# Performance work log

Measured on AMD Instinct MI355X. Metric: run time of the kernel, lower is better.

## Reference

```python
import jax, jax.numpy as jnp
import numpy as np

# Clockwork RNN config (mirrors global args in the original script)
N1, N2, N3 = 16, 8, 8          # len(args.x1/x2/x3)
MULT = 8
DX = N1 + N2 + N3               # 32
D1, D2, D3 = N1*MULT, N2*MULT, N3*MULT  # 128, 64, 64
DH1 = DX * MULT                 # 256
DH2 = 512
DY = 4
T = 192
B = 512
R2, R3 = 2, 4                   # args.x2_rate, args.x3_rate


def _schedule_masks():
    # feat[j]: which input features are consumed at step j (zeroing a feature
    # is equivalent to slicing the matching rows of w_x).
    # blk[j]: which hidden units are updated at step j (others keep old value).
    feat = np.zeros((T, DX), np.float32)
    blk = np.zeros((T, DH1), np.bool_)
    for j in range(T):
        if (j + 1) % R2 == 0:
            if (j + 1) % R3 == 0:
                feat[j, :] = 1.0
                blk[j, :] = True
            else:
                feat[j, :N1 + N2] = 1.0
                blk[j, :D1 + D2] = True
        else:
            feat[j, :N1] = 1.0
            blk[j, :D1] = True
    return jnp.asarray(feat), jnp.asarray(blk)


def setup_inputs() -> dict:
    key = jax.random.key(0)
    ks = jax.random.split(key, 8)
    std = 1.0 / np.sqrt(DH1)
    u = lambda k, shape, s: jax.random.uniform(k, shape, jnp.float32, -s, s)
    return {
        "x": jax.random.normal(ks[0], (B, T, DX), jnp.float32),
        "w_x": u(ks[1], (DY, DX, DH1), std),
        "w_h": u(ks[2], (DY, DH1, DH1), std),
        "b": u(ks[3], (DY, DH1), std),
        "W1": u(ks[4], (DY, DH1, DH2), 1.0 / np.sqrt(DH1)),
        "b1": u(ks[5], (DY, DH2), 1.0 / np.sqrt(DH1)),
        "W2": u(ks[6], (DY, DH2), 1.0 / np.sqrt(DH2)),
        "b2": u(ks[7], (DY,), 1.0 / np.sqrt(DH2)),
    }


def reference(x, w_x, w_h, b, W1, b1, W2, b2):
    feat, blk = _schedule_masks()

    def step(h, inp):
        xj, fm, bm = inp              # xj:[B,DX] fm:[DX] bm:[DH1]
        xin = xj * fm                 # masked features == sliced w_x rows
        cand = jnp.tanh(
            jnp.einsum("bx,yxd->byd", xin, w_x)
            + jnp.einsum("byd,yde->bye", h, w_h)
            + b
        )                             # [B,DY,DH1]
        h = jnp.where(bm, cand, h)    # only scheduled blocks update
        return h, None

    h0 = jnp.zeros((x.shape[0], DY, DH1), x.dtype)
    hT, _ = jax.lax.scan(step, h0, (jnp.swapaxes(x, 0, 1), feat, blk))
    hid = jax.nn.relu(jnp.einsum("byd,ydh->byh", hT, W1) + b1)
    y = jnp.einsum("byh,yh->by", hid, W2) + b2   # [B,DY]
    return y
```

## Files before the change

### kernel.cpp

```cpp
#include <hip/hip_runtime.h>
#include <math.h>


#define TT    192
#define DXX   32
#define DH1   256
#define DH2   512
#define NY    4
#define ROWS8 8
#define PADK  264

typedef _Float16 f16x8 __attribute__((ext_vector_type(8)));
typedef __attribute__((ext_vector_type(4))) float f32x4;
typedef __attribute__((ext_vector_type(2))) int   i32x2;
typedef __attribute__((ext_vector_type(4))) int   i32x4;

template<int N> struct IC { static constexpr int v = N; };

__device__ __forceinline__ unsigned pkrtz(float a, float b) {
    unsigned d;
    asm("v_cvt_pkrtz_f16_f32 %0, %1, %2" : "=v"(d) : "v"(a), "v"(b));
    return d;
}
__device__ __forceinline__ unsigned short f16bits(_Float16 h) {
    union { _Float16 f; unsigned short u; } c; c.f = h; return c.u;
}
__device__ __forceinline__ float fast_tanh(float v) {
    float t = __builtin_amdgcn_exp2f(v * 2.885390081777927f);
    return fmaf(-2.f, __builtin_amdgcn_rcpf(t + 1.f), 1.f);
}

__global__ __launch_bounds__(512, 2) void cwrnn_mfma8(
    const float* __restrict__ x,
    const float* __restrict__ w_x,
    const float* __restrict__ w_h,
    const float* __restrict__ bias,
    const float* __restrict__ W1,
    const float* __restrict__ b1,
    const float* __restrict__ W2,
    const float* __restrict__ b2,
    float* __restrict__ out)
{
    __shared__ _Float16 hb[2][ROWS8 * PADK];
    __shared__ float red[8][ROWS8];
    __shared__ float scratch[DXX * DH1];

    const int t    = threadIdx.x;
    const int lane = t & 63;
    const int w    = t >> 6;
    const int r    = lane & 15;
    const int rb   = r & 7;
    const int q    = lane >> 4;
    const int y    = blockIdx.x & 3;
    const int b0   = (blockIdx.x >> 2) * ROWS8;

    const float* wx_g = w_x + (size_t)y * DXX * DH1;
    const float* wh_g = w_h + (size_t)y * DH1 * DH1;

    for (int i = t; i < ROWS8 * PADK; i += 512) hb[0][i] = (_Float16)0.f;

    f16x8 wxf[2];
    for (int i = t * 4; i < DXX * DH1; i += 2048)
        *(f32x4*)&scratch[i] = *(const f32x4*)&wx_g[i];
    __syncthreads();
    #pragma unroll
    for (int m = 0; m < 2; ++m) {
        f16x8 vh;
        #pragma unroll
        for (int jj = 0; jj < 8; ++jj)
            vh[jj] = (_Float16)scratch[(q * 8 + jj) * DH1 + ((m * 8 + w) << 4) + r];
        wxf[m] = vh;
    }
    __syncthreads();

    f16x8 whf[8][2];
    #pragma unroll
    for (int kt = 0; kt < 8; ++kt) {
        for (int i = t * 4; i < 32 * DH1; i += 2048)
            *(f32x4*)&scratch[i] = *(const f32x4*)&wh_g[kt * 32 * DH1 + i];
        __syncthreads();
        #pragma unroll
        for (int m = 0; m < 2; ++m) {
            f16x8 vh;
            #pragma unroll
            for (int jj = 0; jj < 8; ++jj)
                vh[jj] = (_Float16)scratch[(q * 8 + jj) * DH1 + ((m * 8 + w) << 4) + r];
            whf[kt][m] = vh;
        }
        __syncthreads();
    }

    f32x4 bias4[2];
    #pragma unroll
    for (int m = 0; m < 2; ++m)
        #pragma unroll
        for (int rr = 0; rr < 4; ++rr)
            bias4[m][rr] = bias[y * DH1 + ((m * 8 + w) << 4) + q * 4 + rr];

    const _Float16* hrd[2] = { &hb[0][rb * PADK] + q * 8,
                               &hb[1][rb * PADK] + q * 8 };
    _Float16* hwr[2] = { &hb[0][rb * PADK + w * 16 + q * 4],
                         &hb[1][rb * PADK + w * 16 + q * 4] };

    const float* xrow = x + (size_t)(b0 + rb) * TT * DXX + q * 8;
    f32x4 cxa = *(const f32x4*)&xrow[0];
    f32x4 cxb = *(const f32x4*)&xrow[4];

    auto body = [&](int j, auto SC, int cur) {
        constexpr int S  = SC.v;
        constexpr int NF = (S == 0) ? 16 : (S == 1) ? 24 : 32;
        const bool m1act = (S == 2) || (S == 1 && w < 4);

        const int jn = (j + 1 < TT) ? j + 1 : j;
        const f32x4 pxa = *(const f32x4*)&xrow[jn * DXX];
        const f32x4 pxb = *(const f32x4*)&xrow[jn * DXX + 4];

        f16x8 xf;
        if (q * 8 < NF) {
            union { i32x4 i; f16x8 h; } ux;
            ux.i = (i32x4){ (int)pkrtz(cxa[0], cxa[1]), (int)pkrtz(cxa[2], cxa[3]),
                            (int)pkrtz(cxb[0], cxb[1]), (int)pkrtz(cxb[2], cxb[3]) };
            xf = ux.h;
        } else {
            xf = (f16x8)(_Float16)0.f;
        }

        const _Float16* hp = hrd[cur];

        f32x4 a0a = bias4[0], a0b = {0,0,0,0};
        f32x4 a1a = bias4[1], a1b = {0,0,0,0};

        #pragma unroll
        for (int kt = 0; kt < 4; ++kt) {
            const f16x8 hv0 = *(const f16x8*)(hp + kt * 32);
            const f16x8 hv1 = *(const f16x8*)(hp + (kt + 4) * 32);
            a0a = __builtin_amdgcn_mfma_f32_16x16x32_f16(whf[kt][0], hv0, a0a, 0, 0, 0);
            a0b = __builtin_amdgcn_mfma_f32_16x16x32_f16(whf[kt + 4][0], hv1, a0b, 0, 0, 0);
            if (m1act) {
                a1a = __builtin_amdgcn_mfma_f32_16x16x32_f16(whf[kt][1], hv0, a1a, 0, 0, 0);
                a1b = __builtin_amdgcn_mfma_f32_16x16x32_f16(whf[kt + 4][1], hv1, a1b, 0, 0, 0);
            }
        }
        a0b = __builtin_amdgcn_mfma_f32_16x16x32_f16(wxf[0], xf, a0b, 0, 0, 0);
        if (m1act)
            a1b = __builtin_amdgcn_mfma_f32_16x16x32_f16(wxf[1], xf, a1b, 0, 0, 0);

        {
            const f32x4 s = a0a + a0b;
            const unsigned short h0 = f16bits((_Float16)fast_tanh(s[0]));
            const unsigned short h1 = f16bits((_Float16)fast_tanh(s[1]));
            const unsigned short h2 = f16bits((_Float16)fast_tanh(s[2]));
            const unsigned short h3 = f16bits((_Float16)fast_tanh(s[3]));
            if (r < 8) {
                *(i32x2*)(hwr[cur ^ 1]) =
                    (i32x2){ (int)(h0 | ((unsigned)h1 << 16)),
                             (int)(h2 | ((unsigned)h3 << 16)) };
            }
        }
        if (m1act) {
            const f32x4 s = a1a + a1b;
            const unsigned short h0 = f16bits((_Float16)fast_tanh(s[0]));
            const unsigned short h1 = f16bits((_Float16)fast_tanh(s[1]));
            const unsigned short h2 = f16bits((_Float16)fast_tanh(s[2]));
            const unsigned short h3 = f16bits((_Float16)fast_tanh(s[3]));
            if (r < 8) {
                *(i32x2*)(hwr[cur ^ 1] + 128) =
                    (i32x2){ (int)(h0 | ((unsigned)h1 << 16)),
                             (int)(h2 | ((unsigned)h3 << 16)) };
            }
        } else {
            if (r < 8)
                *(i32x2*)(hwr[cur ^ 1] + 128) = *(const i32x2*)(hwr[cur] + 128);
        }
        __syncthreads();
        cxa = pxa; cxb = pxb;
    };

    for (int j = 0; j < TT; j += 4) {
        body(j + 0, IC<0>{}, 0);
        body(j + 1, IC<1>{}, 1);
        body(j + 2, IC<0>{}, 0);
        body(j + 3, IC<2>{}, 1);
    }

    float* hT = scratch;
    for (int i = t; i < DH1 * ROWS8; i += 512) {
        const int row = i & 7, k = i >> 3;
        hT[k * ROWS8 + row] = (float)hb[0][row * PADK + k];
    }
    __syncthreads();

    const float* W1_g = W1 + (size_t)y * DH1 * DH2;
    float a0[8];
    #pragma unroll
    for (int m = 0; m < 8; ++m) a0[m] = 0.f;
    for (int k = 0; k < DH1; ++k) {
        const float wv = W1_g[(size_t)k * DH2 + t];
        const f32x4 hA = *(const f32x4*)&hT[k * ROWS8];
        const f32x4 hB = *(const f32x4*)&hT[k * ROWS8 + 4];
        a0[0] += hA[0] * wv; a0[1] += hA[1] * wv;
        a0[2] += hA[2] * wv; a0[3] += hA[3] * wv;
        a0[4] += hB[0] * wv; a0[5] += hB[1] * wv;
        a0[6] += hB[2] * wv; a0[7] += hB[3] * wv;
    }
    {
        const float b1v = b1[y * DH2 + t];
        const float w2v = W2[y * DH2 + t];
        float p[8];
        #pragma unroll
        for (int m = 0; m < 8; ++m)
            p[m] = fmaxf(a0[m] + b1v, 0.f) * w2v;
        #pragma unroll
        for (int m = 0; m < 8; ++m) {
            float v = p[m];
            for (int off = 32; off > 0; off >>= 1) v += __shfl_down(v, off);
            if (lane == 0) red[w][m] = v;
        }
    }
    __syncthreads();
    if (t < ROWS8) {
        float s = b2[y];
        #pragma unroll
        for (int ww = 0; ww < 8; ++ww) s += red[ww][t];
        out[(size_t)(b0 + t) * NY + y] = s;
    }
}

extern "C" void kernel_launch(void* const* d_in, const int* in_sizes, int n_in,
                              void* d_out, int out_size, void* d_ws, size_t ws_size,
                              hipStream_t stream) {
    const float* x   = (const float*)d_in[0];
    const float* w_x = (const float*)d_in[1];
    const float* w_h = (const float*)d_in[2];
    const float* b   = (const float*)d_in[3];
    const float* W1  = (const float*)d_in[4];
    const float* b1  = (const float*)d_in[5];
    const float* W2  = (const float*)d_in[6];
    const float* b2  = (const float*)d_in[7];
    float* out = (float*)d_out;

    dim3 grid(256), block(512);
    hipLaunchKernelGGL(cwrnn_mfma8, grid, block, 0, stream,
                       x, w_x, w_h, b, W1, b1, W2, b2, out);
}
```

Measured before the change: 144.7 us.

## Halve batch rows per block to double grid and pack tanh outputs

```diff
diff --git a/kernel.cpp b/kernel.cpp
--- a/kernel.cpp
+++ b/kernel.cpp
@@ -7,7 +7,7 @@
 #define DH1   256
 #define DH2   512
 #define NY    4
-#define ROWS8 8
+#define ROWS4 4
 #define PADK  264
 
 typedef _Float16 f16x8 __attribute__((ext_vector_type(8)));
@@ -30,7 +30,7 @@
     return fmaf(-2.f, __builtin_amdgcn_rcpf(t + 1.f), 1.f);
 }
 
-__global__ __launch_bounds__(512, 2) void cwrnn_mfma8(
+__global__ __launch_bounds__(512, 4) void cwrnn_mfma9(
     const float* __restrict__ x,
     const float* __restrict__ w_x,
     const float* __restrict__ w_h,
@@ -41,23 +41,23 @@
     const float* __restrict__ b2,
     float* __restrict__ out)
 {
-    __shared__ _Float16 hb[2][ROWS8 * PADK];
-    __shared__ float red[8][ROWS8];
+    __shared__ _Float16 hb[2][ROWS4 * PADK];
+    __shared__ float red[8][ROWS4];
     __shared__ float scratch[DXX * DH1];
 
     const int t    = threadIdx.x;
     const int lane = t & 63;
     const int w    = t >> 6;
     const int r    = lane & 15;
-    const int rb   = r & 7;
+    const int rb   = r & 3;
     const int q    = lane >> 4;
     const int y    = blockIdx.x & 3;
-    const int b0   = (blockIdx.x >> 2) * ROWS8;
+    const int b0   = (blockIdx.x >> 2) * ROWS4;
 
     const float* wx_g = w_x + (size_t)y * DXX * DH1;
     const float* wh_g = w_h + (size_t)y * DH1 * DH1;
 
-    for (int i = t; i < ROWS8 * PADK; i += 512) hb[0][i] = (_Float16)0.f;
+    for (int i = t; i < ROWS4 * PADK; i += 512) hb[0][i] = (_Float16)0.f;
 
     f16x8 wxf[2];
     for (int i = t * 4; i < DXX * DH1; i += 2048)
@@ -99,8 +99,10 @@
 
     const _Float16* hrd[2] = { &hb[0][rb * PADK] + q * 8,
                                &hb[1][rb * PADK] + q * 8 };
-    _Float16* hwr[2] = { &hb[0][rb * PADK + w * 16 + q * 4],
-                         &hb[1][rb * PADK + w * 16 + q * 4] };
+    const int tile_off = ((r < 8) ? w : 8 + w) << 4;
+    _Float16* hws[2] = { &hb[0][rb * PADK + tile_off + q * 4],
+                         &hb[1][rb * PADK + tile_off + q * 4] };
+    const bool wlane = ((r & 7) < 4);
 
     const float* xrow = x + (size_t)(b0 + rb) * TT * DXX + q * 8;
     f32x4 cxa = *(const f32x4*)&xrow[0];
@@ -114,6 +116,9 @@
         const int jn = (j + 1 < TT) ? j + 1 : j;
         const f32x4 pxa = *(const f32x4*)&xrow[jn * DXX];
         const f32x4 pxb = *(const f32x4*)&xrow[jn * DXX + 4];
+
+        i32x2 old1;
+        if (!m1act) old1 = *(const i32x2*)(hws[cur]);
 
         f16x8 xf;
         if (q * 8 < NF) {
@@ -146,31 +151,25 @@
             a1b = __builtin_amdgcn_mfma_f32_16x16x32_f16(wxf[1], xf, a1b, 0, 0, 0);
 
         {
-            const f32x4 s = a0a + a0b;
-            const unsigned short h0 = f16bits((_Float16)fast_tanh(s[0]));
-            const unsigned short h1 = f16bits((_Float16)fast_tanh(s[1]));
-            const unsigned short h2 = f16bits((_Float16)fast_tanh(s[2]));
-            const unsigned short h3 = f16bits((_Float16)fast_tanh(s[3]));
-            if (r < 8) {
-                *(i32x2*)(hwr[cur ^ 1]) =
-                    (i32x2){ (int)(h0 | ((unsigned)h1 << 16)),
-                             (int)(h2 | ((unsigned)h3 << 16)) };
+            const f32x4 s0 = a0a + a0b;
+            f32x4 sel;
+            if (m1act) {
+                const f32x4 s1 = a1a + a1b;
+                sel[0] = (r < 8) ? s0[0] : s1[0];
+                sel[1] = (r < 8) ? s0[1] : s1[1];
+                sel[2] = (r < 8) ? s0[2] : s1[2];
+                sel[3] = (r < 8) ? s0[3] : s1[3];
+            } else {
+                sel = s0;
             }
-        }
-        if (m1act) {
-            const f32x4 s = a1a + a1b;
-            const unsigned short h0 = f16bits((_Float16)fast_tanh(s[0]));
-            const unsigned short h1 = f16bits((_Float16)fast_tanh(s[1]));
-            const unsigned short h2 = f16bits((_Float16)fast_tanh(s[2]));
-            const unsigned short h3 = f16bits((_Float16)fast_tanh(s[3]));
-            if (r < 8) {
-                *(i32x2*)(hwr[cur ^ 1] + 128) =
-                    (i32x2){ (int)(h0 | ((unsigned)h1 << 16)),
-                             (int)(h2 | ((unsigned)h3 << 16)) };
-            }
-        } else {
-            if (r < 8)
-                *(i32x2*)(hwr[cur ^ 1] + 128) = *(const i32x2*)(hwr[cur] + 128);
+            const unsigned short h0 = f16bits((_Float16)fast_tanh(sel[0]));
+            const unsigned short h1 = f16bits((_Float16)fast_tanh(sel[1]));
+            const unsigned short h2 = f16bits((_Float16)fast_tanh(sel[2]));
+            const unsigned short h3 = f16bits((_Float16)fast_tanh(sel[3]));
+            i32x2 wv = (i32x2){ (int)(h0 | ((unsigned)h1 << 16)),
+                                (int)(h2 | ((unsigned)h3 << 16)) };
+            if (!m1act && r >= 8) wv = old1;
+            if (wlane) *(i32x2*)(hws[cur ^ 1]) = wv;
         }
         __syncthreads();
         cxa = pxa; cxb = pxb;
@@ -184,41 +183,38 @@
     }
 
     float* hT = scratch;
-    for (int i = t; i < DH1 * ROWS8; i += 512) {
-        const int row = i & 7, k = i >> 3;
-        hT[k * ROWS8 + row] = (float)hb[0][row * PADK + k];
+    for (int i = t; i < DH1 * ROWS4; i += 512) {
+        const int row = i & 3, k = i >> 2;
+        hT[k * ROWS4 + row] = (float)hb[0][row * PADK + k];
     }
     __syncthreads();
 
     const float* W1_g = W1 + (size_t)y * DH1 * DH2;
-    float a0[8];
-    #pragma unroll
-    for (int m = 0; m < 8; ++m) a0[m] = 0.f;
+    float a0[4];
+    #pragma unroll
+    for (int m = 0; m < 4; ++m) a0[m] = 0.f;
     for (int k = 0; k < DH1; ++k) {
         const float wv = W1_g[(size_t)k * DH2 + t];
-        const f32x4 hA = *(const f32x4*)&hT[k * ROWS8];
-        const f32x4 hB = *(const f32x4*)&hT[k * ROWS8 + 4];
+        const f32x4 hA = *(const f32x4*)&hT[k * ROWS4];
         a0[0] += hA[0] * wv; a0[1] += hA[1] * wv;
         a0[2] += hA[2] * wv; a0[3] += hA[3] * wv;
-        a0[4] += hB[0] * wv; a0[5] += hB[1] * wv;
-        a0[6] += hB[2] * wv; a0[7] += hB[3] * wv;
     }
     {
         const float b1v = b1[y * DH2 + t];
         const float w2v = W2[y * DH2 + t];
-        float p[8];
-        #pragma unroll
-        for (int m = 0; m < 8; ++m)
+        float p[4];
+        #pragma unroll
+        for (int m = 0; m < 4; ++m)
             p[m] = fmaxf(a0[m] + b1v, 0.f) * w2v;
         #pragma unroll
-        for (int m = 0; m < 8; ++m) {
+        for (int m = 0; m < 4; ++m) {
             float v = p[m];
             for (int off = 32; off > 0; off >>= 1) v += __shfl_down(v, off);
             if (lane == 0) red[w][m] = v;
         }
     }
     __syncthreads();
-    if (t < ROWS8) {
+    if (t < ROWS4) {
         float s = b2[y];
         #pragma unroll
         for (int ww = 0; ww < 8; ++ww) s += red[ww][t];
@@ -239,7 +235,7 @@
     const float* b2  = (const float*)d_in[7];
     float* out = (float*)d_out;
 
-    dim3 grid(256), block(512);
-    hipLaunchKernelGGL(cwrnn_mfma8, grid, block, 0, stream,
+    dim3 grid(512), block(512);
+    hipLaunchKernelGGL(cwrnn_mfma9, grid, block, 0, stream,
                        x, w_x, w_h, b, W1, b1, W2, b2, out);
 }
```

Result: slower. 214.9 us (+48.5%).

## Split hidden state into separately double-buffered halves with swizzled LDS layout

Applied to the files above, without the earlier changes.

```diff
diff --git a/kernel.cpp b/kernel.cpp
--- a/kernel.cpp
+++ b/kernel.cpp
@@ -8,7 +8,8 @@
 #define DH2   512
 #define NY    4
 #define ROWS8 8
-#define PADK  264
+#define RS    136
+#define BUFS  1088
 
 typedef _Float16 f16x8 __attribute__((ext_vector_type(8)));
 typedef __attribute__((ext_vector_type(4))) float f32x4;
@@ -30,7 +31,7 @@
     return fmaf(-2.f, __builtin_amdgcn_rcpf(t + 1.f), 1.f);
 }
 
-__global__ __launch_bounds__(512, 2) void cwrnn_mfma8(
+__global__ __launch_bounds__(512, 2) void cwrnn_mfma11(
     const float* __restrict__ x,
     const float* __restrict__ w_x,
     const float* __restrict__ w_h,
@@ -41,7 +42,7 @@
     const float* __restrict__ b2,
     float* __restrict__ out)
 {
-    __shared__ _Float16 hb[2][ROWS8 * PADK];
+    __shared__ __align__(16) _Float16 harr[4 * BUFS];
     __shared__ float red[8][ROWS8];
     __shared__ float scratch[DXX * DH1];
 
@@ -57,7 +58,7 @@
     const float* wx_g = w_x + (size_t)y * DXX * DH1;
     const float* wh_g = w_h + (size_t)y * DH1 * DH1;
 
-    for (int i = t; i < ROWS8 * PADK; i += 512) hb[0][i] = (_Float16)0.f;
+    for (int i = t; i < 4 * BUFS; i += 512) harr[i] = (_Float16)0.f;
 
     f16x8 wxf[2];
     for (int i = t * 4; i < DXX * DH1; i += 2048)
@@ -97,17 +98,20 @@
         for (int rr = 0; rr < 4; ++rr)
             bias4[m][rr] = bias[y * DH1 + ((m * 8 + w) << 4) + q * 4 + rr];
 
-    const _Float16* hrd[2] = { &hb[0][rb * PADK] + q * 8,
-                               &hb[1][rb * PADK] + q * 8 };
-    _Float16* hwr[2] = { &hb[0][rb * PADK + w * 16 + q * 4],
-                         &hb[1][rb * PADK + w * 16 + q * 4] };
+    int roff[4];
+    #pragma unroll
+    for (int kt = 0; kt < 4; ++kt)
+        roff[kt] = rb * RS + (((kt + rb) & 3) << 5) + q * 8;
+    const int woff = rb * RS + (((((unsigned)w >> 1) + rb) & 3) << 5)
+                   + ((w & 1) << 4) + (q << 2);
 
     const float* xrow = x + (size_t)(b0 + rb) * TT * DXX + q * 8;
     f32x4 cxa = *(const f32x4*)&xrow[0];
     f32x4 cxb = *(const f32x4*)&xrow[4];
 
-    auto body = [&](int j, auto SC, int cur) {
+    auto body = [&](auto SC, auto RAC, auto RBC, int j) {
         constexpr int S  = SC.v;
+        constexpr int RA = RAC.v, RB = RBC.v;
         constexpr int NF = (S == 0) ? 16 : (S == 1) ? 24 : 32;
         const bool m1act = (S == 2) || (S == 1 && w < 4);
 
@@ -125,15 +129,18 @@
             xf = (f16x8)(_Float16)0.f;
         }
 
-        const _Float16* hp = hrd[cur];
-
-        f32x4 a0a = bias4[0], a0b = {0,0,0,0};
-        f32x4 a1a = bias4[1], a1b = {0,0,0,0};
+        f32x4 a0a = bias4[0];
+        f32x4 a0b = __builtin_amdgcn_mfma_f32_16x16x32_f16(wxf[0], xf,
+                        (f32x4){0.f, 0.f, 0.f, 0.f}, 0, 0, 0);
+        f32x4 a1a = bias4[1];
+        f32x4 a1b = {0.f, 0.f, 0.f, 0.f};
+        if (m1act)
+            a1b = __builtin_amdgcn_mfma_f32_16x16x32_f16(wxf[1], xf, a1b, 0, 0, 0);
 
         #pragma unroll
         for (int kt = 0; kt < 4; ++kt) {
-            const f16x8 hv0 = *(const f16x8*)(hp + kt * 32);
-            const f16x8 hv1 = *(const f16x8*)(hp + (kt + 4) * 32);
+            const f16x8 hv0 = *(const f16x8*)&harr[RA * BUFS + roff[kt]];
+            const f16x8 hv1 = *(const f16x8*)&harr[2 * BUFS + RB * BUFS + roff[kt]];
             a0a = __builtin_amdgcn_mfma_f32_16x16x32_f16(whf[kt][0], hv0, a0a, 0, 0, 0);
             a0b = __builtin_amdgcn_mfma_f32_16x16x32_f16(whf[kt + 4][0], hv1, a0b, 0, 0, 0);
             if (m1act) {
@@ -141,52 +148,85 @@
                 a1b = __builtin_amdgcn_mfma_f32_16x16x32_f16(whf[kt + 4][1], hv1, a1b, 0, 0, 0);
             }
         }
-        a0b = __builtin_amdgcn_mfma_f32_16x16x32_f16(wxf[0], xf, a0b, 0, 0, 0);
-        if (m1act)
-            a1b = __builtin_amdgcn_mfma_f32_16x16x32_f16(wxf[1], xf, a1b, 0, 0, 0);
-
-        {
-            const f32x4 s = a0a + a0b;
-            const unsigned short h0 = f16bits((_Float16)fast_tanh(s[0]));
-            const unsigned short h1 = f16bits((_Float16)fast_tanh(s[1]));
-            const unsigned short h2 = f16bits((_Float16)fast_tanh(s[2]));
-            const unsigned short h3 = f16bits((_Float16)fast_tanh(s[3]));
+
+        const f32x4 s0 = a0a + a0b;
+        if (S == 0) {
             if (r < 8) {
-                *(i32x2*)(hwr[cur ^ 1]) =
+                const unsigned short h0 = f16bits((_Float16)fast_tanh(s0[0]));
+                const unsigned short h1 = f16bits((_Float16)fast_tanh(s0[1]));
+                const unsigned short h2 = f16bits((_Float16)fast_tanh(s0[2]));
+                const unsigned short h3 = f16bits((_Float16)fast_tanh(s0[3]));
+                *(i32x2*)&harr[(RA ^ 1) * BUFS + woff] =
                     (i32x2){ (int)(h0 | ((unsigned)h1 << 16)),
                              (int)(h2 | ((unsigned)h3 << 16)) };
             }
-        }
-        if (m1act) {
-            const f32x4 s = a1a + a1b;
-            const unsigned short h0 = f16bits((_Float16)fast_tanh(s[0]));
-            const unsigned short h1 = f16bits((_Float16)fast_tanh(s[1]));
-            const unsigned short h2 = f16bits((_Float16)fast_tanh(s[2]));
-            const unsigned short h3 = f16bits((_Float16)fast_tanh(s[3]));
-            if (r < 8) {
-                *(i32x2*)(hwr[cur ^ 1] + 128) =
-                    (i32x2){ (int)(h0 | ((unsigned)h1 << 16)),
-                             (int)(h2 | ((unsigned)h3 << 16)) };
+        } else if (S == 2 ) {
+            const f32x4 s1 = a1a + a1b;
+            f32x4 sel;
+            sel[0] = (r < 8) ? s0[0] : s1[0];
+            sel[1] = (r < 8) ? s0[1] : s1[1];
+            sel[2] = (r < 8) ? s0[2] : s1[2];
+            sel[3] = (r < 8) ? s0[3] : s1[3];
+            const unsigned short h0 = f16bits((_Float16)fast_tanh(sel[0]));
+            const unsigned short h1 = f16bits((_Float16)fast_tanh(sel[1]));
+            const unsigned short h2 = f16bits((_Float16)fast_tanh(sel[2]));
+            const unsigned short h3 = f16bits((_Float16)fast_tanh(sel[3]));
+            const int wa = (r < 8) ? (RA ^ 1) * BUFS + woff
+                                   : 2 * BUFS + (RB ^ 1) * BUFS + woff;
+            *(i32x2*)&harr[wa] = (i32x2){ (int)(h0 | ((unsigned)h1 << 16)),
+                                          (int)(h2 | ((unsigned)h3 << 16)) };
+        } else {
+            if (w < 4) {
+                const f32x4 s1 = a1a + a1b;
+                f32x4 sel;
+                sel[0] = (r < 8) ? s0[0] : s1[0];
+                sel[1] = (r < 8) ? s0[1] : s1[1];
+                sel[2] = (r < 8) ? s0[2] : s1[2];
+                sel[3] = (r < 8) ? s0[3] : s1[3];
+                const unsigned short h0 = f16bits((_Float16)fast_tanh(sel[0]));
+                const unsigned short h1 = f16bits((_Float16)fast_tanh(sel[1]));
+                const unsigned short h2 = f16bits((_Float16)fast_tanh(sel[2]));
+                const unsigned short h3 = f16bits((_Float16)fast_tanh(sel[3]));
+                const int wa = (r < 8) ? (RA ^ 1) * BUFS + woff
+                                       : 2 * BUFS + (RB ^ 1) * BUFS + woff;
+                *(i32x2*)&harr[wa] = (i32x2){ (int)(h0 | ((unsigned)h1 << 16)),
+                                              (int)(h2 | ((unsigned)h3 << 16)) };
+            } else {
+                if (r < 8) {
+                    const unsigned short h0 = f16bits((_Float16)fast_tanh(s0[0]));
+                    const unsigned short h1 = f16bits((_Float16)fast_tanh(s0[1]));
+                    const unsigned short h2 = f16bits((_Float16)fast_tanh(s0[2]));
+                    const unsigned short h3 = f16bits((_Float16)fast_tanh(s0[3]));
+                    *(i32x2*)&harr[(RA ^ 1) * BUFS + woff] =
+                        (i32x2){ (int)(h0 | ((unsigned)h1 << 16)),
+                                 (int)(h2 | ((unsigned)h3 << 16)) };
+                } else {
+                    *(i32x2*)&harr[2 * BUFS + (RB ^ 1) * BUFS + woff] =
+                        *(const i32x2*)&harr[2 * BUFS + RB * BUFS + woff];
+                }
             }
-        } else {
-            if (r < 8)
-                *(i32x2*)(hwr[cur ^ 1] + 128) = *(const i32x2*)(hwr[cur] + 128);
         }
         __syncthreads();
         cxa = pxa; cxb = pxb;
     };
 
     for (int j = 0; j < TT; j += 4) {
-        body(j + 0, IC<0>{}, 0);
-        body(j + 1, IC<1>{}, 1);
-        body(j + 2, IC<0>{}, 0);
-        body(j + 3, IC<2>{}, 1);
+        body(IC<0>{}, IC<0>{}, IC<0>{}, j + 0);
+        body(IC<1>{}, IC<1>{}, IC<0>{}, j + 1);
+        body(IC<0>{}, IC<0>{}, IC<1>{}, j + 2);
+        body(IC<2>{}, IC<1>{}, IC<1>{}, j + 3);
     }
 
     float* hT = scratch;
     for (int i = t; i < DH1 * ROWS8; i += 512) {
         const int row = i & 7, k = i >> 3;
-        hT[k * ROWS8 + row] = (float)hb[0][row * PADK + k];
+        float v;
+        if (k < 128)
+            v = (float)harr[row * RS + ((((k >> 5) + row) & 3) << 5) + (k & 31)];
+        else
+            v = (float)harr[2 * BUFS + row * RS
+                            + (((((k - 128) >> 5) + row) & 3) << 5) + (k & 31)];
+        hT[k * ROWS8 + row] = v;
     }
     __syncthreads();
 
@@ -240,6 +280,6 @@
     float* out = (float*)d_out;
 
     dim3 grid(256), block(512);
-    hipLaunchKernelGGL(cwrnn_mfma8, grid, block, 0, stream,
+    hipLaunchKernelGGL(cwrnn_mfma11, grid, block, 0, stream,
                        x, w_x, w_h, b, W1, b1, W2, b2, out);
 }
```

Result: slower. 154.7 us (+6.9%).
